# Optimization experiments

Hardware: AMD Instinct MI355X
Metric: run time of the kernel (lower is better)

The kernel has to match this reference:

```python
import jax, jax.numpy as jnp
import numpy as np

EPS = 1e-5
SCALE = 30.0

def _ln(x, g, b):
    m = jnp.mean(x, axis=-1, keepdims=True)
    v = jnp.mean((x - m) ** 2, axis=-1, keepdims=True)
    return (x - m) * jax.lax.rsqrt(v + EPS) * g + b

def setup_inputs() -> dict:
    key = jax.random.key(0)
    ks = jax.random.split(key, 12)
    B, L, K, H, NIN = 4, 2048, 48, 128, 512
    s = 0.02
    return {
        "h_V": jax.random.normal(ks[0], (B, L, H), jnp.float32),
        "h_E": jax.random.normal(ks[1], (B, L, K, NIN - H), jnp.float32),
        "mask_V": jnp.ones((B, L), jnp.float32),
        "mask_E": jnp.ones((B, L, K), jnp.float32),
        "w1": jax.random.normal(ks[2], (NIN, H), jnp.float32) * s,
        "b1": jnp.zeros((H,), jnp.float32),
        "w2": jax.random.normal(ks[3], (H, H), jnp.float32) * s,
        "b2": jnp.zeros((H,), jnp.float32),
        "w3": jax.random.normal(ks[4], (H, H), jnp.float32) * s,
        "b3": jnp.zeros((H,), jnp.float32),
        "g1": jnp.ones((H,), jnp.float32),
        "bn1": jnp.zeros((H,), jnp.float32),
        "g2": jnp.ones((H,), jnp.float32),
        "bn2": jnp.zeros((H,), jnp.float32),
        "wf1": jax.random.normal(ks[5], (H, 4 * H), jnp.float32) * s,
        "bf1": jnp.zeros((4 * H,), jnp.float32),
        "wf2": jax.random.normal(ks[6], (4 * H, H), jnp.float32) * s,
        "bf2": jnp.zeros((H,), jnp.float32),
    }

def reference(h_V, h_E, mask_V, mask_E, w1, b1, w2, b2, w3, b3, g1, bn1, g2, bn2, wf1, bf1, wf2, bf2):
    B, L, H = h_V.shape
    K = h_E.shape[-2]
    gelu = lambda x: jax.nn.gelu(x, approximate=False)  # torch nn.GELU default (erf)
    # expand source node over K neighbors and concat: (B,L,K,num_in)
    h_V_exp = jnp.broadcast_to(h_V[:, :, None, :], (B, L, K, H))
    h_EV = jnp.concatenate([h_V_exp, h_E], axis=-1)
    h_msg = gelu(jnp.einsum('blki,ih->blkh', h_EV, w1) + b1)
    h_msg = gelu(jnp.einsum('blkh,hj->blkj', h_msg, w2) + b2)
    h_msg = jnp.einsum('blkh,hj->blkj', h_msg, w3) + b3
    h_msg = mask_E[..., None] * h_msg
    dh = jnp.sum(h_msg, axis=-2) / SCALE  # masked sum-aggregate over K
    h = _ln(h_V + dh, g1, bn1)
    dff = jnp.einsum('blh,hf->blf', h, wf1) + bf1
    dff = jnp.einsum('blf,fh->blh', gelu(dff), wf2) + bf2
    h = _ln(h + dff, g2, bn2)
    return mask_V[..., None] * h
```

## Files before the change

kernel.cpp:

```cpp
#include <hip/hip_runtime.h>
#include <hip/hip_bf16.h>


typedef __bf16 bf16x8 __attribute__((ext_vector_type(8)));
typedef __bf16 bf16x4 __attribute__((ext_vector_type(4)));
typedef float f32x4 __attribute__((ext_vector_type(4)));

#define HH 128
#define EE 384
#define KK 48

__device__ __forceinline__ float gelu_f(float x) {
  float x2 = x * x;
  float u = x * (-1.5957691216f - 0.0713548163f * x2);
  float e = __expf(u);
  return __fdividef(x, 1.0f + e);
}

__device__ __forceinline__ bf16x8 cvt8v(f32x4 a, f32x4 b) {
  bf16x8 r;
  #pragma unroll
  for (int i = 0; i < 4; ++i) { r[i] = (__bf16)a[i]; r[i + 4] = (__bf16)b[i]; }
  return r;
}

__device__ __forceinline__ f32x4 mfma16(bf16x8 a, bf16x8 b, f32x4 c) {
  return __builtin_amdgcn_mfma_f32_16x16x32_bf16(a, b, c, 0, 0, 0);
}

__device__ __forceinline__ void gload16(const void* g, void* l) {
  __builtin_amdgcn_global_load_lds(
      (const __attribute__((address_space(1))) void*)g,
      (__attribute__((address_space(3))) void*)l, 16, 0, 0);
}

__global__ void prep_kernel(const float* __restrict__ w1, const float* __restrict__ w2,
                            const float* __restrict__ w3, const float* __restrict__ wf1,
                            const float* __restrict__ wf2, __bf16* __restrict__ out) {
  int idx = blockIdx.x * 256 + threadIdx.x;
  if (idx < 49152) {
    int t = idx & 7, lane = (idx >> 3) & 63, n = (idx >> 9) & 7, kc = idx >> 12;
    int e = kc * 32 + (lane >> 4) * 8 + t, h = n * 16 + (lane & 15);
    out[idx] = (__bf16)w1[(128 + e) * 128 + h];
  } else if (idx < 65536) {
    int u = idx - 49152;
    int t = u & 7, lane = (u >> 3) & 63, n = (u >> 9) & 7, kc = u >> 12;
    int e = kc * 32 + (lane >> 4) * 8 + t, h = n * 16 + (lane & 15);
    out[idx] = (__bf16)w2[e * 128 + h];
  } else if (idx < 81920) {
    int u = idx - 65536;
    int t = u & 7, lane = (u >> 3) & 63, n = (u >> 9) & 7, kc = u >> 12;
    int e = kc * 32 + (lane >> 4) * 8 + t, h = n * 16 + (lane & 15);
    out[idx] = (__bf16)w3[e * 128 + h];
  } else if (idx < 147456) {
    int u = idx - 81920;
    int t = u & 7, lane = (u >> 3) & 63, n = (u >> 9) & 7, kc = (u >> 12) & 3, w = u >> 14;
    int f = w * 128 + n * 16 + (lane & 15), h = kc * 32 + (lane >> 4) * 8 + t;
    out[idx] = (__bf16)wf1[h * 512 + f];
  } else if (idx < 212992) {
    int u = idx - 147456;
    int t = u & 7, lane = (u >> 3) & 63, n = (u >> 9) & 1, kc = (u >> 10) & 15, w = u >> 14;
    int j = w * 32 + n * 16 + (lane & 15), f = kc * 32 + (lane >> 4) * 8 + t;
    out[idx] = (__bf16)wf2[f * 128 + j];
  }
}

__global__ __launch_bounds__(128) void v1_kernel(const float* __restrict__ hV,
                                                 const float* __restrict__ w1,
                                                 const float* __restrict__ b1,
                                                 float* __restrict__ V1) {
  __shared__ __align__(16) float sV[16][128];
  const int tid = threadIdx.x;
  const long p0 = (long)blockIdx.x * 16;
  for (int i = 0; i < 16; ++i) sV[i][tid] = hV[(p0 + i) * HH + tid];
  __syncthreads();
  float acc[16];
  float bb = b1[tid];
  #pragma unroll
  for (int p = 0; p < 16; ++p) acc[p] = bb;
  for (int k = 0; k < 128; k += 4) {
    float wa = w1[(k + 0) * HH + tid];
    float wb = w1[(k + 1) * HH + tid];
    float wc = w1[(k + 2) * HH + tid];
    float wd = w1[(k + 3) * HH + tid];
    #pragma unroll
    for (int p = 0; p < 16; ++p) {
      float4 h4 = *(const float4*)&sV[p][k];
      acc[p] = fmaf(h4.x, wa, fmaf(h4.y, wb, fmaf(h4.z, wc, fmaf(h4.w, wd, acc[p]))));
    }
  }
  #pragma unroll
  for (int p = 0; p < 16; ++p) V1[(p0 + p) * HH + tid] = acc[p];
}

__global__ __launch_bounds__(256, 4) void msg_kernel(
    const float* __restrict__ hE, const float* __restrict__ hV,
    const float* __restrict__ maskE,
    const __bf16* __restrict__ w1f, const __bf16* __restrict__ w2f,
    const __bf16* __restrict__ w3f, const float* __restrict__ V1,
    const float* __restrict__ b2, const float* __restrict__ b3,
    const float* __restrict__ g1, const float* __restrict__ bn1,
    float* __restrict__ outH) {
  __shared__ __align__(16) char sBuf[3][12288];
  __shared__ __align__(16) float sBias[512];
  __shared__ __align__(16) float sPart[4][2];

  const int tid = threadIdx.x;
  const int lane = tid & 63;
  const int w = tid >> 6;
  const int fr = lane & 15;
  const int fg = lane >> 4;
  const long p = blockIdx.x;

  for (int j = tid; j < 512; j += 256) {
    float v;
    if (j < 128) v = b2[j];
    else if (j < 256) v = b3[j - 128];
    else if (j < 384) v = g1[j - 256];
    else v = bn1[j - 384];
    sBias[j] = v;
  }
  __syncthreads();

  const float mk0 = maskE[p * KK + fr];
  const float mk1 = maskE[p * KK + 16 + fr];
  const float mk2 = maskE[p * KK + 32 + fr];

  const char* hEp = (const char*)(hE + p * (long)(KK * EE));
  const int lrow = lane >> 4;
  const int lcb = (lane & 15) * 16;
  const int r0 = (w * 3 + 0) * 4 + lrow;
  const int r1 = (w * 3 + 1) * 4 + lrow;
  const int r2 = (w * 3 + 2) * 4 + lrow;
  const char* srcA0 = hEp + r0 * 1536 + (lcb ^ ((r0 & 7) << 4));
  const char* srcA1 = hEp + r1 * 1536 + (lcb ^ ((r1 & 7) << 4));
  const char* srcA2 = hEp + r2 * 1536 + (lcb ^ ((r2 & 7) << 4));
  const int dst0 = (w * 3 + 0) * 1024;
  const int dst1 = (w * 3 + 1) * 1024;
  const int dst2 = (w * 3 + 2) * 1024;

  const __bf16* b1base = w1f + (2 * w) * 512 + lane * 8;
  const __bf16* b2base = w2f + (2 * w) * 512 + lane * 8;
  const __bf16* b3base = w3f + (2 * w) * 512 + lane * 8;

  const int aswz = (fr & 7) << 4;
  const int hswz = (fr & 7) << 4;
  char* hB = &sBuf[0][0];

  f32x4 acc[3][2];
  #pragma unroll
  for (int m = 0; m < 3; ++m)
    #pragma unroll
    for (int n = 0; n < 2; ++n) acc[m][n] = (f32x4){0.f, 0.f, 0.f, 0.f};

  bf16x8 Bs0[2], Bs1[2], Bs2[2], Bs3[2];

#define STAGE(C, BUF) { \
    gload16(srcA0 + (C) * 256, &sBuf[BUF][0] + dst0); \
    gload16(srcA1 + (C) * 256, &sBuf[BUF][0] + dst1); \
    gload16(srcA2 + (C) * 256, &sBuf[BUF][0] + dst2); }
#define LOADB(SET, BASE, KC) { \
    SET[0] = *(const bf16x8*)((BASE) + (KC) * 4096); \
    SET[1] = *(const bf16x8*)((BASE) + (KC) * 4096 + 256); }
#define WAITV(N) asm volatile("s_waitcnt vmcnt(" #N ")" ::: "memory")
#define BAR      asm volatile("s_barrier" ::: "memory")
#define BARL     asm volatile("s_waitcnt lgkmcnt(0)\ns_barrier" ::: "memory")

#define KSTEP(BUF, KS, SET) { \
    const char* rb_ = &sBuf[BUF][0]; \
    const int cb0_ = ((KS) * 128 + fg * 32) ^ aswz; \
    const int cb1_ = ((KS) * 128 + fg * 32 + 16) ^ aswz; \
    f32x4 x0_ = *(const f32x4*)(rb_ + fr * 256 + cb0_); \
    f32x4 x1_ = *(const f32x4*)(rb_ + fr * 256 + cb1_); \
    f32x4 x2_ = *(const f32x4*)(rb_ + (16 + fr) * 256 + cb0_); \
    f32x4 x3_ = *(const f32x4*)(rb_ + (16 + fr) * 256 + cb1_); \
    f32x4 x4_ = *(const f32x4*)(rb_ + (32 + fr) * 256 + cb0_); \
    f32x4 x5_ = *(const f32x4*)(rb_ + (32 + fr) * 256 + cb1_); \
    bf16x8 af0 = cvt8v(x0_, x1_); \
    bf16x8 af1 = cvt8v(x2_, x3_); \
    bf16x8 af2 = cvt8v(x4_, x5_); \
    acc[0][0] = mfma16(SET[0], af0, acc[0][0]); acc[0][1] = mfma16(SET[1], af0, acc[0][1]); \
    acc[1][0] = mfma16(SET[0], af1, acc[1][0]); acc[1][1] = mfma16(SET[1], af1, acc[1][1]); \
    acc[2][0] = mfma16(SET[0], af2, acc[2][0]); acc[2][1] = mfma16(SET[1], af2, acc[2][1]); }

#define KSTEPH(KS, SET) { \
    const int cb_ = ((KS) * 64 + fg * 16) ^ hswz; \
    bf16x8 af0 = *(const bf16x8*)(hB + fr * 256 + cb_); \
    bf16x8 af1 = *(const bf16x8*)(hB + (16 + fr) * 256 + cb_); \
    bf16x8 af2 = *(const bf16x8*)(hB + (32 + fr) * 256 + cb_); \
    acc[0][0] = mfma16(SET[0], af0, acc[0][0]); acc[0][1] = mfma16(SET[1], af0, acc[0][1]); \
    acc[1][0] = mfma16(SET[0], af1, acc[1][0]); acc[1][1] = mfma16(SET[1], af1, acc[1][1]); \
    acc[2][0] = mfma16(SET[0], af2, acc[2][0]); acc[2][1] = mfma16(SET[1], af2, acc[2][1]); }

#define EPI(BQ0, BQ1) { \
    _Pragma("unroll") for (int m_ = 0; m_ < 3; ++m_) { \
      const int rb_ = (m_ * 16 + fr) * 256; \
      { bf16x4 t_; \
        _Pragma("unroll") for (int j_ = 0; j_ < 4; ++j_) t_[j_] = (__bf16)gelu_f(acc[m_][0][j_] + BQ0[j_]); \
        *(bf16x4*)(hB + rb_ + (((2 * w) * 32 + fg * 8) ^ hswz)) = t_; \
        acc[m_][0] = (f32x4){0.f, 0.f, 0.f, 0.f}; } \
      { bf16x4 t_; \
        _Pragma("unroll") for (int j_ = 0; j_ < 4; ++j_) t_[j_] = (__bf16)gelu_f(acc[m_][1][j_] + BQ1[j_]); \
        *(bf16x4*)(hB + rb_ + (((2 * w + 1) * 32 + fg * 8) ^ hswz)) = t_; \
        acc[m_][1] = (f32x4){0.f, 0.f, 0.f, 0.f}; } } }

  STAGE(0, 0);
  LOADB(Bs0, b1base, 0);
  LOADB(Bs1, b1base, 1);
  STAGE(1, 1);
  LOADB(Bs2, b1base, 2);
  LOADB(Bs3, b1base, 3);

  f32x4 vq0, vq1, hq0, hq1;

  WAITV(7); BAR;
  KSTEP(0, 0, Bs0); LOADB(Bs0, b1base, 4);
  KSTEP(0, 1, Bs1); LOADB(Bs1, b1base, 5);
  STAGE(2, 2);

  WAITV(7); BAR;
  KSTEP(1, 0, Bs2); LOADB(Bs2, b1base, 6);
  KSTEP(1, 1, Bs3); LOADB(Bs3, b1base, 7);
  STAGE(3, 0);

  WAITV(7); BAR;
  KSTEP(2, 0, Bs0); LOADB(Bs0, b1base, 8);
  KSTEP(2, 1, Bs1); LOADB(Bs1, b1base, 9);
  STAGE(4, 1);

  WAITV(7); BAR;
  KSTEP(0, 0, Bs2); LOADB(Bs2, b1base, 10);
  KSTEP(0, 1, Bs3); LOADB(Bs3, b1base, 11);
  STAGE(5, 2);

  WAITV(7); BAR;
  KSTEP(1, 0, Bs0); LOADB(Bs0, b2base, 0);
  vq0 = *(const f32x4*)(V1 + p * HH + (2 * w) * 16 + fg * 4);
  vq1 = *(const f32x4*)(V1 + p * HH + (2 * w + 1) * 16 + fg * 4);
  KSTEP(1, 1, Bs1); LOADB(Bs1, b2base, 1);

  WAITV(6); BAR;
  KSTEP(2, 0, Bs2); LOADB(Bs2, b2base, 2);
  KSTEP(2, 1, Bs3); LOADB(Bs3, b2base, 3);

  WAITV(4);
  EPI(vq0, vq1);
  BARL;

  KSTEPH(0, Bs0); LOADB(Bs0, b3base, 0);
  KSTEPH(1, Bs1); LOADB(Bs1, b3base, 1);
  WAITV(4);
  KSTEPH(2, Bs2); LOADB(Bs2, b3base, 2);
  KSTEPH(3, Bs3); LOADB(Bs3, b3base, 3);
  BARL;
  {
    f32x4 bq0 = *(const f32x4*)(&sBias[(2 * w) * 16 + fg * 4]);
    f32x4 bq1 = *(const f32x4*)(&sBias[(2 * w + 1) * 16 + fg * 4]);
    EPI(bq0, bq1);
  }
  BARL;

  WAITV(6);
  KSTEPH(0, Bs0);
  hq0 = *(const f32x4*)(hV + p * HH + (2 * w) * 16 + fg * 4);
  hq1 = *(const f32x4*)(hV + p * HH + (2 * w + 1) * 16 + fg * 4);
  KSTEPH(1, Bs1);
  WAITV(4);
  KSTEPH(2, Bs2);
  KSTEPH(3, Bs3);

  f32x4 red[2];
  {
    #pragma unroll
    for (int n = 0; n < 2; ++n) {
      f32x4 bq = *(const f32x4*)(&sBias[128 + (2 * w + n) * 16 + fg * 4]);
      red[n] = mk0 * (acc[0][n] + bq) + mk1 * (acc[1][n] + bq) + mk2 * (acc[2][n] + bq);
    }
    #pragma unroll
    for (int off = 1; off <= 8; off <<= 1)
      #pragma unroll
      for (int n = 0; n < 2; ++n)
        #pragma unroll
        for (int j = 0; j < 4; ++j)
          red[n][j] += __shfl_xor(red[n][j], off);
  }

  WAITV(0);
  {
    f32x4 xq[2];
    xq[0] = hq0 + red[0] * (1.f / 30.f);
    xq[1] = hq1 + red[1] * (1.f / 30.f);
    float s = 0.f, t = 0.f;
    #pragma unroll
    for (int n = 0; n < 2; ++n)
      #pragma unroll
      for (int j = 0; j < 4; ++j) { float x = xq[n][j]; s += x; t += x * x; }
    s += __shfl_xor(s, 16); s += __shfl_xor(s, 32);
    t += __shfl_xor(t, 16); t += __shfl_xor(t, 32);
    if (lane == 0) { sPart[w][0] = s; sPart[w][1] = t; }
    BARL;
    float S = sPart[0][0] + sPart[1][0] + sPart[2][0] + sPart[3][0];
    float T = sPart[0][1] + sPart[1][1] + sPart[2][1] + sPart[3][1];
    float mean = S * (1.f / 128.f);
    float var = T * (1.f / 128.f) - mean * mean;
    float rs = rsqrtf(var + 1e-5f);
    if (fr == 0) {
      #pragma unroll
      for (int n = 0; n < 2; ++n) {
        f32x4 gq = *(const f32x4*)(&sBias[256 + (2 * w + n) * 16 + fg * 4]);
        f32x4 bq = *(const f32x4*)(&sBias[384 + (2 * w + n) * 16 + fg * 4]);
        f32x4 o;
        #pragma unroll
        for (int j = 0; j < 4; ++j) o[j] = (xq[n][j] - mean) * rs * gq[j] + bq[j];
        *(f32x4*)(outH + p * HH + (2 * w + n) * 16 + fg * 4) = o;
      }
    }
  }
#undef STAGE
#undef LOADB
#undef WAITV
#undef BAR
#undef BARL
#undef KSTEP
#undef KSTEPH
#undef EPI
}

__global__ __launch_bounds__(256, 2) void ffn_kernel(
    const float* __restrict__ xin, const __bf16* __restrict__ wf1g,
    const float* __restrict__ bf1, const __bf16* __restrict__ wf2g,
    const float* __restrict__ bf2, const float* __restrict__ g2,
    const float* __restrict__ bn2, const float* __restrict__ maskV,
    float* __restrict__ out) {
  __shared__ __align__(16) __bf16 sX[16][136];
  __shared__ __align__(16) __bf16 sH1[16][520];
  __shared__ __align__(16) float sOut[16][132];
  const int tid = threadIdx.x, lane = tid & 63, w = tid >> 6;
  const long row0 = (long)blockIdx.x * 16;
  const int fr = lane & 15, fg = lane >> 4;
  const __bf16* bw1 = wf1g + w * 16384 + lane * 8;
  const __bf16* bw2 = wf2g + w * 16384 + lane * 8;

  {
    int r = tid >> 4, c = (tid & 15) * 8;
    const float* src = xin + (row0 + r) * HH + c;
    f32x4 v0 = *(const f32x4*)src, v1 = *(const f32x4*)(src + 4);
    *(bf16x8*)&sX[r][c] = cvt8v(v0, v1);
  }
  __syncthreads();

  f32x4 a1[8];
  #pragma unroll
  for (int n = 0; n < 8; ++n) a1[n] = (f32x4){0.f, 0.f, 0.f, 0.f};
  #pragma unroll
  for (int kc = 0; kc < 4; ++kc) {
    int k0 = kc * 32;
    bf16x8 af0 = *(const bf16x8*)&sX[fr][k0 + fg * 8];
    #pragma unroll
    for (int n = 0; n < 8; ++n) {
      bf16x8 bfr = *(const bf16x8*)(bw1 + (kc * 8 + n) * 512);
      a1[n] = mfma16(af0, bfr, a1[n]);
    }
  }
  #pragma unroll
  for (int n = 0; n < 8; ++n) {
    float bv = bf1[w * 128 + n * 16 + fr];
    #pragma unroll
    for (int j = 0; j < 4; ++j)
      sH1[fg * 4 + j][w * 128 + n * 16 + fr] = (__bf16)gelu_f(a1[n][j] + bv);
  }
  __syncthreads();

  f32x4 a2[2];
  #pragma unroll
  for (int n = 0; n < 2; ++n) a2[n] = (f32x4){0.f, 0.f, 0.f, 0.f};
  #pragma unroll
  for (int kc = 0; kc < 16; ++kc) {
    int k0 = kc * 32;
    bf16x8 af0 = *(const bf16x8*)&sH1[fr][k0 + fg * 8];
    #pragma unroll
    for (int n = 0; n < 2; ++n) {
      bf16x8 bfr = *(const bf16x8*)(bw2 + (kc * 2 + n) * 512);
      a2[n] = mfma16(af0, bfr, a2[n]);
    }
  }
  #pragma unroll
  for (int n = 0; n < 2; ++n) {
    float bv = bf2[w * 32 + n * 16 + fr];
    #pragma unroll
    for (int j = 0; j < 4; ++j)
      sOut[fg * 4 + j][w * 32 + n * 16 + fr] = a2[n][j] + bv;
  }
  __syncthreads();

  {
    int r = tid >> 4, c0 = (tid & 15) * 8;
    long p = row0 + r;
    const float* xp = xin + p * HH + c0;
    float x[8];
    #pragma unroll
    for (int i = 0; i < 8; ++i) x[i] = xp[i] + sOut[r][c0 + i];
    float s = 0.f;
    #pragma unroll
    for (int i = 0; i < 8; ++i) s += x[i];
    s += __shfl_xor(s, 1); s += __shfl_xor(s, 2); s += __shfl_xor(s, 4); s += __shfl_xor(s, 8);
    float mean = s * (1.f / 128.f);
    float q = 0.f;
    #pragma unroll
    for (int i = 0; i < 8; ++i) { float e = x[i] - mean; q += e * e; }
    q += __shfl_xor(q, 1); q += __shfl_xor(q, 2); q += __shfl_xor(q, 4); q += __shfl_xor(q, 8);
    float rs = rsqrtf(q * (1.f / 128.f) + 1e-5f);
    float mv = maskV[p];
    float* op = out + p * HH + c0;
    #pragma unroll
    for (int i = 0; i < 8; ++i)
      op[i] = ((x[i] - mean) * rs * g2[c0 + i] + bn2[c0 + i]) * mv;
  }
}

extern "C" void kernel_launch(void* const* d_in, const int* in_sizes, int n_in,
                              void* d_out, int out_size, void* d_ws, size_t ws_size,
                              hipStream_t stream) {
  const float* hV    = (const float*)d_in[0];
  const float* hE    = (const float*)d_in[1];
  const float* maskV = (const float*)d_in[2];
  const float* maskE = (const float*)d_in[3];
  const float* w1    = (const float*)d_in[4];
  const float* b1    = (const float*)d_in[5];
  const float* w2    = (const float*)d_in[6];
  const float* b2    = (const float*)d_in[7];
  const float* w3    = (const float*)d_in[8];
  const float* b3    = (const float*)d_in[9];
  const float* g1    = (const float*)d_in[10];
  const float* bn1   = (const float*)d_in[11];
  const float* g2    = (const float*)d_in[12];
  const float* bn2   = (const float*)d_in[13];
  const float* wf1   = (const float*)d_in[14];
  const float* bf1   = (const float*)d_in[15];
  const float* wf2   = (const float*)d_in[16];
  const float* bf2   = (const float*)d_in[17];
  float* out = (float*)d_out;

  __bf16* wsb = (__bf16*)d_ws;
  float* V1   = (float*)((char*)d_ws + 425984);
  float* hbuf = (float*)((char*)d_ws + 4620288);

  prep_kernel<<<832, 256, 0, stream>>>(w1, w2, w3, wf1, wf2, wsb);
  v1_kernel<<<512, 128, 0, stream>>>(hV, w1, b1, V1);
  msg_kernel<<<8192, 256, 0, stream>>>(hE, hV, maskE,
                                       wsb, wsb + 49152, wsb + 65536, V1,
                                       b2, b3, g1, bn1, hbuf);
  ffn_kernel<<<512, 256, 0, stream>>>(hbuf, wsb + 81920, bf1, wsb + 147456, bf2,
                                      g2, bn2, maskV, out);
}
```

Baseline: 204.1 us.

## Stage h_E in 128-column chunks with fewer pipeline stages in message kernel

Doubles the per-stage LDS chunk of h_E from 64 to 128 fp32 columns, so layer 1 runs in three stages of four k-steps each instead of six stages of two. Each stage now issues six 16-byte loads per lane, and the wait counts and barriers are reworked to match. This halves the number of barrier and wait points in the first GEMM. In exchange it uses twice the LDS (about 72 KB) and lowers the launch-bounds occupancy hint from 4 to 2 blocks, reducing latency hiding across blocks.

Result: slower. 222.6 us (+9.0%).

```diff
diff --git a/kernel.cpp b/kernel.cpp
--- a/kernel.cpp
+++ b/kernel.cpp
@@ -93,7 +93,7 @@
   for (int p = 0; p < 16; ++p) V1[(p0 + p) * HH + tid] = acc[p];
 }
 
-__global__ __launch_bounds__(256, 4) void msg_kernel(
+__global__ __launch_bounds__(256, 2) void msg_kernel(
     const float* __restrict__ hE, const float* __restrict__ hV,
     const float* __restrict__ maskE,
     const __bf16* __restrict__ w1f, const __bf16* __restrict__ w2f,
@@ -101,7 +101,7 @@
     const float* __restrict__ b2, const float* __restrict__ b3,
     const float* __restrict__ g1, const float* __restrict__ bn1,
     float* __restrict__ outH) {
-  __shared__ __align__(16) char sBuf[3][12288];
+  __shared__ __align__(16) char sBuf[3][24576];
   __shared__ __align__(16) float sBias[512];
   __shared__ __align__(16) float sPart[4][2];
 
@@ -127,17 +127,16 @@
   const float mk2 = maskE[p * KK + 32 + fr];
 
   const char* hEp = (const char*)(hE + p * (long)(KK * EE));
-  const int lrow = lane >> 4;
-  const int lcb = (lane & 15) * 16;
-  const int r0 = (w * 3 + 0) * 4 + lrow;
-  const int r1 = (w * 3 + 1) * 4 + lrow;
-  const int r2 = (w * 3 + 2) * 4 + lrow;
-  const char* srcA0 = hEp + r0 * 1536 + (lcb ^ ((r0 & 7) << 4));
-  const char* srcA1 = hEp + r1 * 1536 + (lcb ^ ((r1 & 7) << 4));
-  const char* srcA2 = hEp + r2 * 1536 + (lcb ^ ((r2 & 7) << 4));
-  const int dst0 = (w * 3 + 0) * 1024;
-  const int dst1 = (w * 3 + 1) * 1024;
-  const int dst2 = (w * 3 + 2) * 1024;
+  const int rhalf = lane >> 5;
+  const int gcol = (lane & 31) * 16;
+  const char* srcR[6];
+  int dstR[6];
+  #pragma unroll
+  for (int g = 0; g < 6; ++g) {
+    int row = w * 12 + 2 * g + rhalf;
+    srcR[g] = hEp + row * 1536 + (gcol ^ ((row & 7) << 4));
+    dstR[g] = (w * 12 + 2 * g) * 512;
+  }
 
   const __bf16* b1base = w1f + (2 * w) * 512 + lane * 8;
   const __bf16* b2base = w2f + (2 * w) * 512 + lane * 8;
@@ -156,9 +155,8 @@
   bf16x8 Bs0[2], Bs1[2], Bs2[2], Bs3[2];
 
 #define STAGE(C, BUF) { \
-    gload16(srcA0 + (C) * 256, &sBuf[BUF][0] + dst0); \
-    gload16(srcA1 + (C) * 256, &sBuf[BUF][0] + dst1); \
-    gload16(srcA2 + (C) * 256, &sBuf[BUF][0] + dst2); }
+    _Pragma("unroll") for (int g_ = 0; g_ < 6; ++g_) \
+      gload16(srcR[g_] + (C) * 512, &sBuf[BUF][0] + dstR[g_]); }
 #define LOADB(SET, BASE, KC) { \
     SET[0] = *(const bf16x8*)((BASE) + (KC) * 4096); \
     SET[1] = *(const bf16x8*)((BASE) + (KC) * 4096 + 256); }
@@ -170,12 +168,12 @@
     const char* rb_ = &sBuf[BUF][0]; \
     const int cb0_ = ((KS) * 128 + fg * 32) ^ aswz; \
     const int cb1_ = ((KS) * 128 + fg * 32 + 16) ^ aswz; \
-    f32x4 x0_ = *(const f32x4*)(rb_ + fr * 256 + cb0_); \
-    f32x4 x1_ = *(const f32x4*)(rb_ + fr * 256 + cb1_); \
-    f32x4 x2_ = *(const f32x4*)(rb_ + (16 + fr) * 256 + cb0_); \
-    f32x4 x3_ = *(const f32x4*)(rb_ + (16 + fr) * 256 + cb1_); \
-    f32x4 x4_ = *(const f32x4*)(rb_ + (32 + fr) * 256 + cb0_); \
-    f32x4 x5_ = *(const f32x4*)(rb_ + (32 + fr) * 256 + cb1_); \
+    f32x4 x0_ = *(const f32x4*)(rb_ + fr * 512 + cb0_); \
+    f32x4 x1_ = *(const f32x4*)(rb_ + fr * 512 + cb1_); \
+    f32x4 x2_ = *(const f32x4*)(rb_ + (16 + fr) * 512 + cb0_); \
+    f32x4 x3_ = *(const f32x4*)(rb_ + (16 + fr) * 512 + cb1_); \
+    f32x4 x4_ = *(const f32x4*)(rb_ + (32 + fr) * 512 + cb0_); \
+    f32x4 x5_ = *(const f32x4*)(rb_ + (32 + fr) * 512 + cb1_); \
     bf16x8 af0 = cvt8v(x0_, x1_); \
     bf16x8 af1 = cvt8v(x2_, x3_); \
     bf16x8 af2 = cvt8v(x4_, x5_); \
@@ -207,50 +205,44 @@
   STAGE(0, 0);
   LOADB(Bs0, b1base, 0);
   LOADB(Bs1, b1base, 1);
-  STAGE(1, 1);
   LOADB(Bs2, b1base, 2);
   LOADB(Bs3, b1base, 3);
+  STAGE(1, 1);
 
   f32x4 vq0, vq1, hq0, hq1;
 
-  WAITV(7); BAR;
+  WAITV(6); BAR;
   KSTEP(0, 0, Bs0); LOADB(Bs0, b1base, 4);
   KSTEP(0, 1, Bs1); LOADB(Bs1, b1base, 5);
+  KSTEP(0, 2, Bs2); LOADB(Bs2, b1base, 6);
+  KSTEP(0, 3, Bs3); LOADB(Bs3, b1base, 7);
   STAGE(2, 2);
 
-  WAITV(7); BAR;
-  KSTEP(1, 0, Bs2); LOADB(Bs2, b1base, 6);
-  KSTEP(1, 1, Bs3); LOADB(Bs3, b1base, 7);
-  STAGE(3, 0);
-
-  WAITV(7); BAR;
-  KSTEP(2, 0, Bs0); LOADB(Bs0, b1base, 8);
-  KSTEP(2, 1, Bs1); LOADB(Bs1, b1base, 9);
-  STAGE(4, 1);
-
-  WAITV(7); BAR;
-  KSTEP(0, 0, Bs2); LOADB(Bs2, b1base, 10);
-  KSTEP(0, 1, Bs3); LOADB(Bs3, b1base, 11);
-  STAGE(5, 2);
-
-  WAITV(7); BAR;
-  KSTEP(1, 0, Bs0); LOADB(Bs0, b2base, 0);
+  WAITV(6); BAR;
+  KSTEP(1, 0, Bs0); LOADB(Bs0, b1base, 8);
+  KSTEP(1, 1, Bs1); LOADB(Bs1, b1base, 9);
+  KSTEP(1, 2, Bs2); LOADB(Bs2, b1base, 10);
+  KSTEP(1, 3, Bs3); LOADB(Bs3, b1base, 11);
   vq0 = *(const f32x4*)(V1 + p * HH + (2 * w) * 16 + fg * 4);
   vq1 = *(const f32x4*)(V1 + p * HH + (2 * w + 1) * 16 + fg * 4);
-  KSTEP(1, 1, Bs1); LOADB(Bs1, b2base, 1);
-
-  WAITV(6); BAR;
-  KSTEP(2, 0, Bs2); LOADB(Bs2, b2base, 2);
-  KSTEP(2, 1, Bs3); LOADB(Bs3, b2base, 3);
-
-  WAITV(4);
+
+  WAITV(2); BAR;
+  KSTEP(2, 0, Bs0); LOADB(Bs0, b2base, 0);
+  KSTEP(2, 1, Bs1); LOADB(Bs1, b2base, 1);
+  KSTEP(2, 2, Bs2); LOADB(Bs2, b2base, 2);
+  KSTEP(2, 3, Bs3); LOADB(Bs3, b2base, 3);
+
+  WAITV(8);
   EPI(vq0, vq1);
   BARL;
 
+  WAITV(6);
   KSTEPH(0, Bs0); LOADB(Bs0, b3base, 0);
+  WAITV(6);
   KSTEPH(1, Bs1); LOADB(Bs1, b3base, 1);
-  WAITV(4);
+  WAITV(6);
   KSTEPH(2, Bs2); LOADB(Bs2, b3base, 2);
+  WAITV(6);
   KSTEPH(3, Bs3); LOADB(Bs3, b3base, 3);
   BARL;
   {
@@ -264,9 +256,11 @@
   KSTEPH(0, Bs0);
   hq0 = *(const f32x4*)(hV + p * HH + (2 * w) * 16 + fg * 4);
   hq1 = *(const f32x4*)(hV + p * HH + (2 * w + 1) * 16 + fg * 4);
+  WAITV(6);
   KSTEPH(1, Bs1);
   WAITV(4);
   KSTEPH(2, Bs2);
+  WAITV(2);
   KSTEPH(3, Bs3);
 
   f32x4 red[2];
```
